# Performance work log

Measured on AMD Instinct MI355X. Metric: run time of the kernel, lower is better.

Reference implementation:

```python
import jax, jax.numpy as jnp
import numpy as np

B, LQ, LK = 8, 1024, 1024
DQ, DK, DV = 1024, 1024, 1024
H = 16
DEPTH = DQ // H  # 64


def setup_inputs() -> dict:
    key = jax.random.key(0)
    ks = jax.random.split(key, 6)
    query = jax.random.normal(ks[0], (B, LQ, DQ), dtype=jnp.float32)
    keys = jax.random.normal(ks[1], (B, LK, DK), dtype=jnp.float32)
    values = jax.random.normal(ks[2], (B, LK, DV), dtype=jnp.float32)
    # Per-head Linear weights (torch Linear: y = x @ W.T, W is [depth, in_dim]);
    # stacked across heads -> [H, depth, in_dim].
    Wq = jax.random.normal(ks[3], (H, DEPTH, DQ), dtype=jnp.float32) / np.sqrt(DQ).astype(np.float32)
    Wk = jax.random.normal(ks[4], (H, DEPTH, DK), dtype=jnp.float32) / np.sqrt(DK).astype(np.float32)
    Wv = jax.random.normal(ks[5], (H, DEPTH, DV), dtype=jnp.float32) / np.sqrt(DV).astype(np.float32)
    return {"query": query, "keys": keys, "values": values, "Wq": Wq, "Wk": Wk, "Wv": Wv}


def reference(query, keys, values, Wq, Wk, Wv):
    depth = Wq.shape[1]
    # Fused per-head projections (replaces the Python loop of small GEMMs)
    q = jnp.einsum('bld,hed->bhle', query, Wq)   # [B,H,Lq,depth]
    k = jnp.einsum('bsd,hed->bhse', keys, Wk)    # [B,H,Lk,depth]
    v = jnp.einsum('bsd,hed->bhse', values, Wv)  # [B,H,Lk,depth]
    scale = jnp.asarray(1.0 / np.sqrt(depth), dtype=q.dtype)
    scores = jnp.einsum('bhle,bhse->bhls', q, k) * scale  # [B,H,Lq,Lk]
    weights = jax.nn.softmax(scores, axis=-1)
    out = jnp.einsum('bhls,bhse->bhle', weights, v)       # [B,H,Lq,depth]
    bsz = query.shape[0]
    # transpose(1,2) then flatten -> [B, Lq*H*depth]
    return out.transpose(0, 2, 1, 3).reshape(bsz, -1)
```

## Files before the change

### kernel.cpp

```cpp
#include <hip/hip_runtime.h>


typedef __attribute__((ext_vector_type(8))) short short8;
typedef __attribute__((ext_vector_type(4))) float f32x4;

typedef const void __attribute__((address_space(1)))* gas_cvptr;
typedef void __attribute__((address_space(3)))* las_vptr;

__device__ __forceinline__ void gll16(const void* g, void* l) {
  __builtin_amdgcn_global_load_lds((gas_cvptr)g, (las_vptr)l, 16, 0, 0);
}

__device__ __forceinline__ unsigned short f2bf(float f) {
  unsigned u = __builtin_bit_cast(unsigned, f);
  u += 0x7fffu + ((u >> 16) & 1u);
  return (unsigned short)(u >> 16);
}

__device__ __forceinline__ unsigned pack2bf(float a, float b) {
  unsigned ua = __builtin_bit_cast(unsigned, a) + 0x8000u;
  unsigned ub = __builtin_bit_cast(unsigned, b) + 0x8000u;
  return (ua >> 16) | (ub & 0xffff0000u);
}

__device__ __forceinline__ float fexp2(float x) {
#if __has_builtin(__builtin_amdgcn_exp2f)
  return __builtin_amdgcn_exp2f(x);
#else
  return exp2f(x);
#endif
}

#define SCALE_L2E 0.18033688011112042f
__global__ void cvt_all(const float* __restrict__ q, const float* __restrict__ k,
                        const float* __restrict__ v, const float* __restrict__ wq,
                        const float* __restrict__ wk, const float* __restrict__ wv,
                        unsigned short* __restrict__ out) {
  long e = ((long)blockIdx.x * 256 + threadIdx.x) * 8;
  const float* src;
  float scale = 1.0f;
  if (e < 25165824) {
    src = (e < 8388608) ? q + e : (e < 16777216) ? k + (e - 8388608) : v + (e - 16777216);
  } else if (e < 26214400) {
    src = wq + (e - 25165824); scale = SCALE_L2E;
  } else if (e < 27262976) {
    src = wk + (e - 26214400);
  } else {
    src = wv + (e - 27262976);
  }
  float4 a = ((const float4*)src)[0], b = ((const float4*)src)[1];
  short8 o;
  o[0] = (short)f2bf(a.x * scale); o[1] = (short)f2bf(a.y * scale);
  o[2] = (short)f2bf(a.z * scale); o[3] = (short)f2bf(a.w * scale);
  o[4] = (short)f2bf(b.x * scale); o[5] = (short)f2bf(b.y * scale);
  o[6] = (short)f2bf(b.z * scale); o[7] = (short)f2bf(b.w * scale);
  *(short8*)(out + e) = o;
}

__global__ __launch_bounds__(256, 2) void proj_gemm(
    const unsigned short* __restrict__ A,
    const unsigned short* __restrict__ Bt,
    unsigned short* __restrict__ Cp) {
  __shared__ unsigned short sAB[2 * 128 * 64];
  unsigned short* sA = sAB;
  unsigned short* sB = sAB + 8192;

  const int tid = threadIdx.x;
  const int lane = tid & 63, wv = tid >> 6;
  const int quad = lane >> 4, l16 = lane & 15;
  const int wm = wv >> 1, wn = wv & 1;
  const int m0 = blockIdx.y * 128, n0 = blockIdx.x * 128;

  f32x4 acc[4][4];
  const f32x4 zero = {0.f, 0.f, 0.f, 0.f};
#pragma unroll
  for (int i = 0; i < 4; ++i)
#pragma unroll
    for (int j = 0; j < 4; ++j) acc[i][j] = zero;

  for (int kt = 0; kt < 16; ++kt) {
    const unsigned short* Ag = A + (size_t)m0 * 1024 + kt * 64;
    const unsigned short* Bg = Bt + (size_t)n0 * 1024 + kt * 64;
#pragma unroll
    for (int i = 0; i < 4; ++i) {
      int c = tid + i * 256;
      int row = c >> 3, cc = (c & 7) * 8;
      gll16(Ag + (size_t)row * 1024 + cc, (char*)sA + c * 16);
      gll16(Bg + (size_t)row * 1024 + cc, (char*)sB + c * 16);
    }
    __syncthreads();
#pragma unroll
    for (int ks = 0; ks < 2; ++ks) {
      short8 af[4], bf[4];
#pragma unroll
      for (int t = 0; t < 4; ++t) {
        af[t] = *(const short8*)(sA + (wm * 64 + t * 16 + l16) * 64 + ks * 32 + quad * 8);
        bf[t] = *(const short8*)(sB + (wn * 64 + t * 16 + l16) * 64 + ks * 32 + quad * 8);
      }
#pragma unroll
      for (int mt = 0; mt < 4; ++mt)
#pragma unroll
        for (int nt = 0; nt < 4; ++nt)
          acc[mt][nt] = __builtin_amdgcn_mfma_f32_16x16x32_bf16(
              af[mt], bf[nt], acc[mt][nt], 0, 0, 0);
    }
    __syncthreads();
  }

  unsigned short* sC = sAB;
#pragma unroll
  for (int mt = 0; mt < 4; ++mt)
#pragma unroll
    for (int nt = 0; nt < 4; ++nt)
#pragma unroll
      for (int r = 0; r < 4; ++r)
        sC[wn * 8192 + (wm * 64 + mt * 16 + quad * 4 + r) * 64 + nt * 16 + l16] =
            f2bf(acc[mt][nt][r]);
  __syncthreads();
  const int h0 = blockIdx.x * 2;
  const int bb = m0 >> 10, l0 = m0 & 1023;
  const size_t base = (((size_t)(bb * 16 + h0)) * 1024 + l0) * 64;
#pragma unroll
  for (int i = 0; i < 8; ++i) {
    int ch = tid + i * 256;
    int hh = ch >> 10, inner = (ch & 1023) * 8;
    *(short8*)(Cp + base + (size_t)hh * 65536 + inner) =
        *(const short8*)(sC + hh * 8192 + inner);
  }
}

__global__ __launch_bounds__(256, 3) void attn(
    const unsigned short* __restrict__ qp,
    const unsigned short* __restrict__ kp,
    const unsigned short* __restrict__ vp,
    float* __restrict__ out) {
  __shared__ unsigned short sQ[128 * 64];
  __shared__ unsigned short sK[64 * 64];
  __shared__ unsigned short sV[64 * 64];
  __shared__ unsigned short sP[4][32 * 72];

  const int tid = threadIdx.x;
  const int lane = tid & 63, wv = tid >> 6;
  const int quad = lane >> 4, l16 = lane & 15;
  const int bh = blockIdx.x;
  const int qt = blockIdx.y;
  const int b = bh >> 4, h = bh & 15;

  const unsigned short* Qg = qp + ((size_t)bh * 1024 + qt * 128) * 64;
  const unsigned short* Kg = kp + (size_t)bh * 65536;
  const unsigned short* Vg = vp + (size_t)bh * 65536;
  unsigned short* sPw = sP[wv];

#pragma unroll
  for (int i = 0; i < 4; ++i) {
    int c = tid + i * 256;
    gll16(Qg + c * 8, (char*)sQ + c * 16);
  }

  const f32x4 zero = {0.f, 0.f, 0.f, 0.f};
  f32x4 oaccT[4][2];
  float lsum[2] = {0.f, 0.f};
#pragma unroll
  for (int et = 0; et < 4; ++et)
#pragma unroll
    for (int qc = 0; qc < 2; ++qc) oaccT[et][qc] = zero;

  for (int kt = 0; kt < 16; ++kt) {
    __syncthreads();
#pragma unroll
    for (int i = 0; i < 2; ++i) {
      int c = tid + i * 256;
      gll16(Kg + (size_t)kt * 4096 + c * 8, (char*)sK + c * 16);
    }
#pragma unroll
    for (int i = 0; i < 2; ++i) {
      int c = tid + i * 256;
      int s = c & 63, e0 = (c >> 6) * 8;
      short8 vv = *(const short8*)(Vg + (size_t)kt * 4096 + s * 64 + e0);
#pragma unroll
      for (int j = 0; j < 8; ++j) sV[(e0 + j) * 64 + s] = (unsigned short)vv[j];
    }
    __syncthreads();

    f32x4 sacc[4][2];
#pragma unroll
    for (int st = 0; st < 4; ++st)
#pragma unroll
      for (int qc = 0; qc < 2; ++qc) sacc[st][qc] = zero;
#pragma unroll
    for (int ks = 0; ks < 2; ++ks) {
      short8 kf[4], qf[2];
#pragma unroll
      for (int st = 0; st < 4; ++st)
        kf[st] = *(const short8*)(sK + (st * 16 + l16) * 64 + ks * 32 + quad * 8);
#pragma unroll
      for (int qc = 0; qc < 2; ++qc)
        qf[qc] = *(const short8*)(sQ + (wv * 32 + qc * 16 + l16) * 64 + ks * 32 + quad * 8);
#pragma unroll
      for (int st = 0; st < 4; ++st)
#pragma unroll
        for (int qc = 0; qc < 2; ++qc)
          sacc[st][qc] = __builtin_amdgcn_mfma_f32_16x16x32_bf16(
              kf[st], qf[qc], sacc[st][qc], 0, 0, 0);
    }

#pragma unroll
    for (int st = 0; st < 4; ++st)
#pragma unroll
      for (int qc = 0; qc < 2; ++qc) {
        float p0 = fexp2(sacc[st][qc][0]);
        float p1 = fexp2(sacc[st][qc][1]);
        float p2 = fexp2(sacc[st][qc][2]);
        float p3 = fexp2(sacc[st][qc][3]);
        lsum[qc] += (p0 + p1) + (p2 + p3);
        uint2 pk;
        pk.x = pack2bf(p0, p1);
        pk.y = pack2bf(p2, p3);
        *(uint2*)(sPw + (qc * 16 + l16) * 72 + st * 16 + quad * 4) = pk;
      }

#pragma unroll
    for (int ks = 0; ks < 2; ++ks) {
      short8 vf[4], pf[2];
#pragma unroll
      for (int et = 0; et < 4; ++et)
        vf[et] = *(const short8*)(sV + (et * 16 + l16) * 64 + ks * 32 + quad * 8);
#pragma unroll
      for (int qc = 0; qc < 2; ++qc)
        pf[qc] = *(const short8*)(sPw + (qc * 16 + l16) * 72 + ks * 32 + quad * 8);
#pragma unroll
      for (int et = 0; et < 4; ++et)
#pragma unroll
        for (int qc = 0; qc < 2; ++qc)
          oaccT[et][qc] = __builtin_amdgcn_mfma_f32_16x16x32_bf16(
              vf[et], pf[qc], oaccT[et][qc], 0, 0, 0);
    }
  }

  float inv[2];
#pragma unroll
  for (int qc = 0; qc < 2; ++qc) {
    float l = lsum[qc];
    l += __shfl_xor(l, 16);
    l += __shfl_xor(l, 32);
    inv[qc] = 1.0f / l;
  }

#pragma unroll
  for (int et = 0; et < 4; ++et)
#pragma unroll
    for (int qc = 0; qc < 2; ++qc) {
      int qg = qt * 128 + wv * 32 + qc * 16 + l16;
      int e0 = et * 16 + quad * 4;
      float4 o;
      o.x = oaccT[et][qc][0] * inv[qc];
      o.y = oaccT[et][qc][1] * inv[qc];
      o.z = oaccT[et][qc][2] * inv[qc];
      o.w = oaccT[et][qc][3] * inv[qc];
      *(float4*)(out + ((size_t)b << 20) + (size_t)qg * 1024 + h * 64 + e0) = o;
    }
}

extern "C" void kernel_launch(void* const* d_in, const int* in_sizes, int n_in,
                              void* d_out, int out_size, void* d_ws, size_t ws_size,
                              hipStream_t stream) {
  const float* q  = (const float*)d_in[0];
  const float* k  = (const float*)d_in[1];
  const float* v  = (const float*)d_in[2];
  const float* wq = (const float*)d_in[3];
  const float* wk = (const float*)d_in[4];
  const float* wv = (const float*)d_in[5];
  float* out = (float*)d_out;

  const size_t E = (size_t)8 * 1024 * 1024;
  const size_t W = (size_t)16 * 64 * 1024;
  const size_t need = (6 * E + 3 * W) * sizeof(unsigned short);
  if (ws_size < need) return;

  unsigned short* ws  = (unsigned short*)d_ws;
  unsigned short* xq  = ws;
  unsigned short* xk  = ws + E;
  unsigned short* xv  = ws + 2 * E;
  unsigned short* bwq = ws + 3 * E;
  unsigned short* bwk = ws + 3 * E + W;
  unsigned short* bwv = ws + 3 * E + 2 * W;
  unsigned short* qp  = ws + 3 * E + 3 * W;
  unsigned short* kp  = qp + E;
  unsigned short* vp  = qp + 2 * E;

  cvt_all<<<dim3((unsigned)((3 * E + 3 * W) / 2048)), 256, 0, stream>>>(
      q, k, v, wq, wk, wv, ws);

  dim3 gg(8, 64);
  proj_gemm<<<gg, 256, 0, stream>>>(xq, bwq, qp);
  proj_gemm<<<gg, 256, 0, stream>>>(xk, bwk, kp);
  proj_gemm<<<gg, 256, 0, stream>>>(xv, bwv, vp);

  dim3 ga(128, 8);
  attn<<<ga, 256, 0, stream>>>(qp, kp, vp, out);
}
```

Baseline: 315.2 us.

## Swizzle LDS layouts, pre-transpose V in projection, merge projection launches

```diff
diff --git a/kernel.cpp b/kernel.cpp
--- a/kernel.cpp
+++ b/kernel.cpp
@@ -58,18 +58,26 @@
 }
 
 __global__ __launch_bounds__(256, 2) void proj_gemm(
-    const unsigned short* __restrict__ A,
-    const unsigned short* __restrict__ Bt,
-    unsigned short* __restrict__ Cp) {
+    const unsigned short* __restrict__ xq, const unsigned short* __restrict__ xk,
+    const unsigned short* __restrict__ xv, const unsigned short* __restrict__ bwq,
+    const unsigned short* __restrict__ bwk, const unsigned short* __restrict__ bwv,
+    unsigned short* __restrict__ qp, unsigned short* __restrict__ kp,
+    unsigned short* __restrict__ vpT) {
   __shared__ unsigned short sAB[2 * 128 * 64];
   unsigned short* sA = sAB;
   unsigned short* sB = sAB + 8192;
+
+  const int z = blockIdx.z;
+  const unsigned short* A  = z == 0 ? xq  : z == 1 ? xk  : xv;
+  const unsigned short* Bt = z == 0 ? bwq : z == 1 ? bwk : bwv;
+  unsigned short* Cp       = z == 0 ? qp  : z == 1 ? kp  : vpT;
 
   const int tid = threadIdx.x;
   const int lane = tid & 63, wv = tid >> 6;
   const int quad = lane >> 4, l16 = lane & 15;
   const int wm = wv >> 1, wn = wv & 1;
   const int m0 = blockIdx.y * 128, n0 = blockIdx.x * 128;
+  const int key = l16 & 7;
 
   f32x4 acc[4][4];
   const f32x4 zero = {0.f, 0.f, 0.f, 0.f};
@@ -84,18 +92,20 @@
 #pragma unroll
     for (int i = 0; i < 4; ++i) {
       int c = tid + i * 256;
-      int row = c >> 3, cc = (c & 7) * 8;
-      gll16(Ag + (size_t)row * 1024 + cc, (char*)sA + c * 16);
-      gll16(Bg + (size_t)row * 1024 + cc, (char*)sB + c * 16);
+      int row = c >> 3, cp = c & 7;
+      int col = (cp ^ (row & 7)) * 8;
+      gll16(Ag + (size_t)row * 1024 + col, (char*)sA + c * 16);
+      gll16(Bg + (size_t)row * 1024 + col, (char*)sB + c * 16);
     }
     __syncthreads();
 #pragma unroll
     for (int ks = 0; ks < 2; ++ks) {
       short8 af[4], bf[4];
+      const int sw = ((ks * 4 + quad) ^ key) * 8;
 #pragma unroll
       for (int t = 0; t < 4; ++t) {
-        af[t] = *(const short8*)(sA + (wm * 64 + t * 16 + l16) * 64 + ks * 32 + quad * 8);
-        bf[t] = *(const short8*)(sB + (wn * 64 + t * 16 + l16) * 64 + ks * 32 + quad * 8);
+        af[t] = *(const short8*)(sA + (wm * 64 + t * 16 + l16) * 64 + sw);
+        bf[t] = *(const short8*)(sB + (wn * 64 + t * 16 + l16) * 64 + sw);
       }
 #pragma unroll
       for (int mt = 0; mt < 4; ++mt)
@@ -108,36 +118,60 @@
   }
 
   unsigned short* sC = sAB;
-#pragma unroll
-  for (int mt = 0; mt < 4; ++mt)
-#pragma unroll
-    for (int nt = 0; nt < 4; ++nt)
-#pragma unroll
-      for (int r = 0; r < 4; ++r)
-        sC[wn * 8192 + (wm * 64 + mt * 16 + quad * 4 + r) * 64 + nt * 16 + l16] =
-            f2bf(acc[mt][nt][r]);
-  __syncthreads();
   const int h0 = blockIdx.x * 2;
   const int bb = m0 >> 10, l0 = m0 & 1023;
-  const size_t base = (((size_t)(bb * 16 + h0)) * 1024 + l0) * 64;
-#pragma unroll
-  for (int i = 0; i < 8; ++i) {
-    int ch = tid + i * 256;
-    int hh = ch >> 10, inner = (ch & 1023) * 8;
-    *(short8*)(Cp + base + (size_t)hh * 65536 + inner) =
-        *(const short8*)(sC + hh * 8192 + inner);
+  if (z != 2) {
+#pragma unroll
+    for (int mt = 0; mt < 4; ++mt)
+#pragma unroll
+      for (int nt = 0; nt < 4; ++nt)
+#pragma unroll
+        for (int r = 0; r < 4; ++r)
+          sC[wn * 8192 + (wm * 64 + mt * 16 + quad * 4 + r) * 64 + nt * 16 + l16] =
+              f2bf(acc[mt][nt][r]);
+    __syncthreads();
+    const size_t base = (((size_t)(bb * 16 + h0)) * 1024 + l0) * 64;
+#pragma unroll
+    for (int i = 0; i < 8; ++i) {
+      int ch = tid + i * 256;
+      int hh = ch >> 10, inner = (ch & 1023) * 8;
+      *(short8*)(Cp + base + (size_t)hh * 65536 + inner) =
+          *(const short8*)(sC + hh * 8192 + inner);
+    }
+  } else {
+#pragma unroll
+    for (int mt = 0; mt < 4; ++mt)
+#pragma unroll
+      for (int nt = 0; nt < 4; ++nt)
+#pragma unroll
+        for (int r = 0; r < 4; ++r) {
+          int rowIdx = wn * 64 + nt * 16 + l16;
+          int l = wm * 64 + mt * 16 + quad * 4 + r;
+          sC[rowIdx * 128 + (((l >> 3) ^ (rowIdx & 15)) << 3) + (l & 7)] =
+              f2bf(acc[mt][nt][r]);
+        }
+    __syncthreads();
+#pragma unroll
+    for (int i = 0; i < 8; ++i) {
+      int ch = tid + i * 256;
+      int hh = ch >> 10, x = ch & 1023;
+      int e = x >> 4, c = x & 15;
+      int rowIdx = hh * 64 + e;
+      short8 val = *(const short8*)(sC + rowIdx * 128 + ((c ^ (rowIdx & 15)) << 3));
+      *(short8*)(Cp + ((size_t)(bb * 16 + h0 + hh) << 16) + (size_t)e * 1024 + l0 + c * 8) = val;
+    }
   }
 }
 
 __global__ __launch_bounds__(256, 3) void attn(
     const unsigned short* __restrict__ qp,
     const unsigned short* __restrict__ kp,
-    const unsigned short* __restrict__ vp,
+    const unsigned short* __restrict__ vpT,
     float* __restrict__ out) {
   __shared__ unsigned short sQ[128 * 64];
   __shared__ unsigned short sK[64 * 64];
   __shared__ unsigned short sV[64 * 64];
-  __shared__ unsigned short sP[4][32 * 72];
+  __shared__ unsigned short sP[4][32 * 64];
 
   const int tid = threadIdx.x;
   const int lane = tid & 63, wv = tid >> 6;
@@ -145,16 +179,18 @@
   const int bh = blockIdx.x;
   const int qt = blockIdx.y;
   const int b = bh >> 4, h = bh & 15;
+  const int key = l16 & 7;
 
   const unsigned short* Qg = qp + ((size_t)bh * 1024 + qt * 128) * 64;
   const unsigned short* Kg = kp + (size_t)bh * 65536;
-  const unsigned short* Vg = vp + (size_t)bh * 65536;
+  const unsigned short* Vg = vpT + (size_t)bh * 65536;
   unsigned short* sPw = sP[wv];
 
 #pragma unroll
   for (int i = 0; i < 4; ++i) {
     int c = tid + i * 256;
-    gll16(Qg + c * 8, (char*)sQ + c * 16);
+    int row = c >> 3, cp = c & 7;
+    gll16(Qg + row * 64 + ((cp ^ (row & 7)) * 8), (char*)sQ + c * 16);
   }
 
   const f32x4 zero = {0.f, 0.f, 0.f, 0.f};
@@ -170,15 +206,11 @@
 #pragma unroll
     for (int i = 0; i < 2; ++i) {
       int c = tid + i * 256;
-      gll16(Kg + (size_t)kt * 4096 + c * 8, (char*)sK + c * 16);
-    }
-#pragma unroll
-    for (int i = 0; i < 2; ++i) {
-      int c = tid + i * 256;
-      int s = c & 63, e0 = (c >> 6) * 8;
-      short8 vv = *(const short8*)(Vg + (size_t)kt * 4096 + s * 64 + e0);
-#pragma unroll
-      for (int j = 0; j < 8; ++j) sV[(e0 + j) * 64 + s] = (unsigned short)vv[j];
+      int row = c >> 3, cp = c & 7;
+      gll16(Kg + (size_t)kt * 4096 + row * 64 + ((cp ^ (row & 7)) * 8),
+            (char*)sK + c * 16);
+      gll16(Vg + (size_t)row * 1024 + kt * 64 + ((cp ^ (row & 7)) * 8),
+            (char*)sV + c * 16);
     }
     __syncthreads();
 
@@ -190,12 +222,13 @@
 #pragma unroll
     for (int ks = 0; ks < 2; ++ks) {
       short8 kf[4], qf[2];
+      const int sw = ((ks * 4 + quad) ^ key) * 8;
 #pragma unroll
       for (int st = 0; st < 4; ++st)
-        kf[st] = *(const short8*)(sK + (st * 16 + l16) * 64 + ks * 32 + quad * 8);
+        kf[st] = *(const short8*)(sK + (st * 16 + l16) * 64 + sw);
 #pragma unroll
       for (int qc = 0; qc < 2; ++qc)
-        qf[qc] = *(const short8*)(sQ + (wv * 32 + qc * 16 + l16) * 64 + ks * 32 + quad * 8);
+        qf[qc] = *(const short8*)(sQ + (wv * 32 + qc * 16 + l16) * 64 + sw);
 #pragma unroll
       for (int st = 0; st < 4; ++st)
 #pragma unroll
@@ -216,18 +249,21 @@
         uint2 pk;
         pk.x = pack2bf(p0, p1);
         pk.y = pack2bf(p2, p3);
-        *(uint2*)(sPw + (qc * 16 + l16) * 72 + st * 16 + quad * 4) = pk;
+        int up = (st * 4 + quad) ^ (key << 1);
+        *(uint2*)(sPw + (qc * 16 + l16) * 64 + up * 4) = pk;
       }
 
 #pragma unroll
     for (int ks = 0; ks < 2; ++ks) {
       short8 vf[4], pf[2];
+      const int sw = ((ks * 4 + quad) ^ key) * 8;
+      const int swp = ((ks * 8 + quad * 2) ^ (key << 1)) * 4;
 #pragma unroll
       for (int et = 0; et < 4; ++et)
-        vf[et] = *(const short8*)(sV + (et * 16 + l16) * 64 + ks * 32 + quad * 8);
+        vf[et] = *(const short8*)(sV + (et * 16 + l16) * 64 + sw);
 #pragma unroll
       for (int qc = 0; qc < 2; ++qc)
-        pf[qc] = *(const short8*)(sPw + (qc * 16 + l16) * 72 + ks * 32 + quad * 8);
+        pf[qc] = *(const short8*)(sPw + (qc * 16 + l16) * 64 + swp);
 #pragma unroll
       for (int et = 0; et < 4; ++et)
 #pragma unroll
@@ -286,16 +322,13 @@
   unsigned short* bwv = ws + 3 * E + 2 * W;
   unsigned short* qp  = ws + 3 * E + 3 * W;
   unsigned short* kp  = qp + E;
-  unsigned short* vp  = qp + 2 * E;
+  unsigned short* vpT = qp + 2 * E;
 
   cvt_all<<<dim3((unsigned)((3 * E + 3 * W) / 2048)), 256, 0, stream>>>(
       q, k, v, wq, wk, wv, ws);
 
-  dim3 gg(8, 64);
-  proj_gemm<<<gg, 256, 0, stream>>>(xq, bwq, qp);
-  proj_gemm<<<gg, 256, 0, stream>>>(xk, bwk, kp);
-  proj_gemm<<<gg, 256, 0, stream>>>(xv, bwv, vp);
-
-  dim3 ga(128, 8);
-  attn<<<ga, 256, 0, stream>>>(qp, kp, vp, out);
-}
+  proj_gemm<<<dim3(8, 64, 3), 256, 0, stream>>>(xq, xk, xv, bwq, bwk, bwv,
+                                                qp, kp, vpT);
+
+  attn<<<dim3(128, 8), 256, 0, stream>>>(qp, kp, vpT, out);
+}
```

Measured after the change: 276.7 us. -12.2%, faster.
